# Kernel tuning notes

Hardware: AMD Instinct MI355X
Metric: run time of the kernel (lower is better)

Reference implementation:

```python
import jax, jax.numpy as jnp
import numpy as np

B, S, D, H, DK = 32, 1024, 256, 8, 32
MASK_VALUE = -1e-30  # note: NOT -inf; masked scores become ~0 pre-softmax, faithful to source


def setup_inputs() -> dict:
    key = jax.random.key(0)
    ks = jax.random.split(key, 7)
    query = jax.random.normal(ks[0], (B, S, D), dtype=jnp.float32)
    key_t = jax.random.normal(ks[1], (B, S, D), dtype=jnp.float32)
    value = jax.random.normal(ks[2], (B, S, D), dtype=jnp.float32)
    # binary observation mask over key positions
    mask = (jax.random.uniform(ks[3], (B, S)) > 0.5).astype(jnp.float32)
    glorot = jax.nn.initializers.glorot_uniform(in_axis=1, out_axis=2)
    Wq = glorot(ks[4], (H, D, DK), jnp.float32)
    Wk = glorot(ks[5], (H, D, DK), jnp.float32)
    Wv = glorot(ks[6], (H, D, DK), jnp.float32)
    return {"query": query, "key": key_t, "value": value, "mask": mask,
            "Wq": Wq, "Wk": Wk, "Wv": Wv}


def reference(query, key, value, mask, Wq, Wk, Wv):
    # per-head projections, vectorized over heads: [B,S,D] x [H,D,DK] -> [B,H,S,DK]
    q = jnp.einsum('bsd,hdk->bhsk', query, Wq)
    k = jnp.einsum('bsd,hdk->bhsk', key, Wk)
    v = jnp.einsum('bsd,hdk->bhsk', value, Wv)
    # raw scores (no 1/sqrt(dk) scaling in source): [B,H,Sq,Sk]
    A = jnp.einsum('bhqk,bhsk->bhqs', q, k)
    m = mask[:, None, None, :]  # [B,1,1,Sk]
    A = m * A + (1.0 - m) * MASK_VALUE  # multiplicative mask, NOT additive
    A = jax.nn.softmax(A, axis=-1)
    out = jnp.einsum('bhqs,bhsk->bhqk', A, v)  # [B,H,Sq,DK]
    # concat heads along last dim, matching torch.cat order
    return out.transpose(0, 2, 1, 3).reshape(B, S, H * DK)
```

## Files before the change

### kernel.cpp

```cpp
#include <hip/hip_runtime.h>
#include <math.h>

#define B_  32
#define S_  1024
#define D_  256
#define H_  8
#define DK_ 32
#define MASKV (-1e-30f)
#define LOG2E 1.44269504f

typedef __attribute__((ext_vector_type(4))) short bf4_t;
typedef __attribute__((ext_vector_type(8))) short bf8_t;
typedef __attribute__((ext_vector_type(4))) float f4_t;

__device__ __forceinline__ unsigned fbits(float x) {
    union { float f; unsigned u; } v; v.f = x; return v.u;
}
__device__ __forceinline__ float bitsf(unsigned u) {
    union { unsigned u; float f; } v; v.u = u; return v.f;
}

#if __has_builtin(__builtin_amdgcn_exp2f)
#define EXP2F(x) __builtin_amdgcn_exp2f(x)
#else
#define EXP2F(x) __expf((x) * 0.69314718f)
#endif

__device__ __forceinline__ void gld16(const void* g, void* l) {
    __builtin_amdgcn_global_load_lds(
        (const __attribute__((address_space(1))) void*)g,
        (__attribute__((address_space(3))) void*)l, 16, 0, 0);
}

#define PSEL 0x07060302u


__global__ __launch_bounds__(256) void prep_w(
    const float* __restrict__ Wq, const float* __restrict__ Wk,
    const float* __restrict__ Wv, short* __restrict__ WpH, short* __restrict__ WpL)
{
    const int a = blockIdx.x >> 3;
    const int h = blockIdx.x & 7;
    const float* W = (a == 0 ? Wq : (a == 1 ? Wk : Wv)) + (size_t)h * 256 * 32;
    const int t = threadIdx.x;
    const int k    = t & 31;
    const int dgrp = t >> 5;
    const int ng   = h * 2 + (k >> 4);
    const int l15  = k & 15;
#pragma unroll
    for (int jj = blockIdx.y * 2; jj < blockIdx.y * 2 + 2; ++jj) {
        const int d0 = jj * 32 + dgrp * 4;
        float x[4];
#pragma unroll
        for (int r = 0; r < 4; ++r) x[r] = W[(size_t)(d0 + r) * 32 + k];
        unsigned hu[4], lu[4];
#pragma unroll
        for (int r = 0; r < 4; ++r) {
            unsigned hb = (fbits(x[r]) + 0x8000u) & 0xFFFF0000u;
            hu[r] = hb;
            lu[r] = fbits(x[r] - bitsf(hb)) + 0x8000u;
        }
        uint2 hp = make_uint2(__builtin_amdgcn_perm(hu[1], hu[0], PSEL),
                              __builtin_amdgcn_perm(hu[3], hu[2], PSEL));
        uint2 lp = make_uint2(__builtin_amdgcn_perm(lu[1], lu[0], PSEL),
                              __builtin_amdgcn_perm(lu[3], lu[2], PSEL));
        const int quad = (d0 >> 3) & 3;
        const int jb   = d0 & 7;
        size_t off = (size_t)a * 65536
                   + ((size_t)(jj * 16 + ng) * 64 + quad * 16 + l15) * 8 + jb;
        *(uint2*)&WpH[off] = hp;
        *(uint2*)&WpL[off] = lp;
    }
}

__global__ __launch_bounds__(256) void proj_kernel(
    const float* __restrict__ Xq, const float* __restrict__ Xk,
    const float* __restrict__ Xv, const float* __restrict__ mask,
    const short* __restrict__ WpH, const short* __restrict__ WpL,
    short* __restrict__ qpH, short* __restrict__ qpL,
    short* __restrict__ kpH, short* __restrict__ kpL,
    short* __restrict__ vpT)
{
    __shared__ __align__(16) short XsH[8192];
    __shared__ __align__(16) short XsL[8192];

    const int a  = blockIdx.y;
    const float* X = (a == 0 ? Xq : (a == 1 ? Xk : Xv));
    const short* WH = WpH + (size_t)a * 65536;
    const short* WL = WpL + (size_t)a * 65536;
    const int m0 = blockIdx.x * 64;

    const int tid  = threadIdx.x;
    const int lane = tid & 63;
    const int wv   = tid >> 6;
    const int l15  = lane & 15;
    const int quad = lane >> 4;

    f4_t acc[4][4];
#pragma unroll
    for (int i = 0; i < 4; ++i)
#pragma unroll
        for (int j = 0; j < 4; ++j) acc[i][j] = (f4_t){0.f, 0.f, 0.f, 0.f};

    const int r    = tid >> 2;
    const int dseg = tid & 3;
    const int tix  = r >> 4;
    const int rl15 = r & 15;

    for (int h2 = 0; h2 < 2; ++h2) {
        __syncthreads();
        {
            const float* xp = X + (size_t)(m0 + r) * 256 + h2 * 128 + dseg * 32;
#pragma unroll
            for (int q = 0; q < 4; ++q) {
                float4 x0 = *(const float4*)(xp + q * 8);
                float4 x1 = *(const float4*)(xp + q * 8 + 4);
                float xv[8] = {x0.x, x0.y, x0.z, x0.w, x1.x, x1.y, x1.z, x1.w};
                bf8_t hi, lo;
#pragma unroll
                for (int j = 0; j < 8; ++j) {
                    unsigned hu = (fbits(xv[j]) + 0x8000u) & 0xFFFF0000u;
                    hi[j] = (short)(hu >> 16);
                    lo[j] = (short)((fbits(xv[j] - bitsf(hu)) + 0x8000u) >> 16);
                }
                const int off = ((dseg * 4 + tix) * 64 + q * 16 + rl15) * 8;
                *(bf8_t*)&XsH[off] = hi;
                *(bf8_t*)&XsL[off] = lo;
            }
        }
        __syncthreads();

#pragma unroll
        for (int kcl = 0; kcl < 4; ++kcl) {
            const int kc = h2 * 4 + kcl;
            bf8_t xH[4], xL[4];
#pragma unroll
            for (int t = 0; t < 4; ++t) {
                xH[t] = *(const bf8_t*)&XsH[((kcl * 4 + t) * 64 + lane) * 8];
                xL[t] = *(const bf8_t*)&XsL[((kcl * 4 + t) * 64 + lane) * 8];
            }
#pragma unroll
            for (int ns = 0; ns < 4; ++ns) {
                const size_t wo = ((size_t)(kc * 16 + wv * 4 + ns) * 64 + lane) * 8;
                bf8_t wh = *(const bf8_t*)&WH[wo];
                bf8_t wl = *(const bf8_t*)&WL[wo];
#pragma unroll
                for (int t = 0; t < 4; ++t) {
                    f4_t c = acc[t][ns];
                    if (a < 2) {
                        c = __builtin_amdgcn_mfma_f32_16x16x32_bf16(wh, xH[t], c, 0, 0, 0);
                        c = __builtin_amdgcn_mfma_f32_16x16x32_bf16(wl, xH[t], c, 0, 0, 0);
                        c = __builtin_amdgcn_mfma_f32_16x16x32_bf16(wh, xL[t], c, 0, 0, 0);
                    } else {
                        c = __builtin_amdgcn_mfma_f32_16x16x32_bf16(xH[t], wh, c, 0, 0, 0);
                        c = __builtin_amdgcn_mfma_f32_16x16x32_bf16(xH[t], wl, c, 0, 0, 0);
                        c = __builtin_amdgcn_mfma_f32_16x16x32_bf16(xL[t], wh, c, 0, 0, 0);
                    }
                    acc[t][ns] = c;
                }
            }
        }
    }

    const int b  = m0 >> 10;
    const int sB = m0 & 1023;
    if (a < 2) {
        short* dH = (a == 0) ? qpH : kpH;
        short* dL = (a == 0) ? qpL : kpL;
        const float* mbp = mask + (size_t)b * 1024;
#pragma unroll
        for (int t = 0; t < 4; ++t) {
            const int s = sB + t * 16 + l15;
            const float scale = (a == 0) ? LOG2E : mbp[s];
            const int grp = (sB >> 4) + t;
#pragma unroll
            for (int ns = 0; ns < 4; ++ns) {
                const int h_    = wv * 2 + (ns >> 1);
                const int quadA = (ns & 1) * 2 + (quad >> 1);
                const int jb    = (quad & 1) * 4;
                unsigned hu[4], lu[4];
#pragma unroll
                for (int rr = 0; rr < 4; ++rr) {
                    float x = acc[t][ns][rr] * scale;
                    unsigned h32 = fbits(x) + 0x8000u;
                    hu[rr] = h32;
                    float hf = bitsf(h32 & 0xFFFF0000u);
                    lu[rr] = fbits(x - hf) + 0x8000u;
                }
                uint2 hp = make_uint2(__builtin_amdgcn_perm(hu[1], hu[0], PSEL),
                                      __builtin_amdgcn_perm(hu[3], hu[2], PSEL));
                uint2 lp = make_uint2(__builtin_amdgcn_perm(lu[1], lu[0], PSEL),
                                      __builtin_amdgcn_perm(lu[3], lu[2], PSEL));
                size_t off = (((size_t)(b * 8 + h_) * 64 + grp) * 64
                              + quadA * 16 + l15) * 8 + jb;
                *(uint2*)&dH[off] = hp;
                *(uint2*)&dL[off] = lp;
            }
        }
    } else {
#pragma unroll
        for (int t = 0; t < 4; ++t) {
            int sr = sB + t * 16 + quad * 4;
#pragma unroll
            for (int ns = 0; ns < 4; ++ns) {
                int n = wv * 64 + ns * 16 + l15;
                int h = n >> 5, k = n & 31;
                unsigned eu[4];
#pragma unroll
                for (int rr = 0; rr < 4; ++rr) eu[rr] = fbits(acc[t][ns][rr]) + 0x8000u;
                uint2 pk = make_uint2(__builtin_amdgcn_perm(eu[1], eu[0], PSEL),
                                      __builtin_amdgcn_perm(eu[3], eu[2], PSEL));
                *(uint2*)&vpT[((size_t)(b * 8 + h) * 32 + k) * 1024 + sr] = pk;
            }
        }
    }
}

__global__ __launch_bounds__(256) void attn_kernel(
    const short* __restrict__ qpH, const short* __restrict__ qpL,
    const short* __restrict__ kpH, const short* __restrict__ kpL,
    const short* __restrict__ vpT, float* __restrict__ out)
{
    __shared__ __align__(16) short KsH[2][2048];
    __shared__ __align__(16) short KsL[2][2048];
    __shared__ __align__(16) short VsT[2][32 * 72];

    const int tid  = threadIdx.x;
    const int lane = tid & 63;
    const int wv   = tid >> 6;
    const int l15  = lane & 15;
    const int quad = lane >> 4;

    const int L  = (blockIdx.z * gridDim.y + blockIdx.y) * gridDim.x + blockIdx.x;
    const int li = L >> 3;
    const int bh = (L & 7) * 32 + (li >> 3);
    const int qt = li & 7;
    const int b  = bh >> 3;
    const int h  = bh & 7;
    const int woff = qt * 128 + wv * 32;

    bf8_t qh[2], ql[2];
#pragma unroll
    for (int qs = 0; qs < 2; ++qs) {
        const int grp = qt * 8 + wv * 2 + qs;
        size_t off = (((size_t)bh * 64 + grp) * 64 + lane) * 8;
        qh[qs] = *(const bf8_t*)&qpH[off];
        ql[qs] = *(const bf8_t*)&qpL[off];
    }

    f4_t accO[2][2];
    f4_t accS[2];
#pragma unroll
    for (int i = 0; i < 2; ++i) {
        accS[i] = (f4_t){0.f, 0.f, 0.f, 0.f};
#pragma unroll
        for (int j = 0; j < 2; ++j) accO[i][j] = (f4_t){0.f, 0.f, 0.f, 0.f};
    }
    const bf4_t ones4 = {(short)0x3F80, (short)0x3F80, (short)0x3F80, (short)0x3F80};

    const int dv = tid >> 3, seg = tid & 7;

    {
        size_t toff = ((size_t)bh * 64) * 512;
        gld16(kpH + toff + wv * 512 + lane * 8, (char*)KsH[0] + wv * 1024);
        gld16(kpL + toff + wv * 512 + lane * 8, (char*)KsL[0] + wv * 1024);
        uint4 v0 = *(const uint4*)&vpT[((size_t)bh * 32 + dv) * 1024 + seg * 8];
        *(uint4*)&VsT[0][dv * 72 + seg * 8] = v0;
    }
    __syncthreads();

    int cur = 0;
    for (int kt = 0; kt < 16; ++kt) {
        const int nxt = cur ^ 1;

        uint4 vreg;
        if (kt < 15) {
            size_t toff = ((size_t)bh * 64 + (kt + 1) * 4) * 512;
            gld16(kpH + toff + wv * 512 + lane * 8, (char*)KsH[nxt] + wv * 1024);
            gld16(kpL + toff + wv * 512 + lane * 8, (char*)KsL[nxt] + wv * 1024);
            vreg = *(const uint4*)&vpT[((size_t)bh * 32 + dv) * 1024 + (kt + 1) * 64 + seg * 8];
        }

        __builtin_amdgcn_s_setprio(1);
        f4_t sc[2][4];
#pragma unroll
        for (int ks = 0; ks < 4; ++ks) {
            bf8_t kh = *(const bf8_t*)&KsH[cur][ks * 512 + lane * 8];
            bf8_t kl = *(const bf8_t*)&KsL[cur][ks * 512 + lane * 8];
#pragma unroll
            for (int qs = 0; qs < 2; ++qs) {
                f4_t c = __builtin_amdgcn_mfma_f32_16x16x32_bf16(kh, qh[qs],
                             (f4_t){0.f, 0.f, 0.f, 0.f}, 0, 0, 0);
                c = __builtin_amdgcn_mfma_f32_16x16x32_bf16(kl, qh[qs], c, 0, 0, 0);
                c = __builtin_amdgcn_mfma_f32_16x16x32_bf16(kh, ql[qs], c, 0, 0, 0);
                sc[qs][ks] = c;
            }
        }

        bf4_t pf[2][4];
#pragma unroll
        for (int ks = 0; ks < 4; ++ks) {
#pragma unroll
            for (int qs = 0; qs < 2; ++qs) {
                unsigned eu[4];
#pragma unroll
                for (int r = 0; r < 4; ++r)
                    eu[r] = fbits(EXP2F(sc[qs][ks][r])) + 0x8000u;
                union { uint2 u; bf4_t v; } cv;
                cv.u = make_uint2(__builtin_amdgcn_perm(eu[1], eu[0], PSEL),
                                  __builtin_amdgcn_perm(eu[3], eu[2], PSEL));
                pf[qs][ks] = cv.v;
            }
        }

#pragma unroll
        for (int ks = 0; ks < 4; ++ks) {
            bf4_t vf0 = *(const bf4_t*)&VsT[cur][l15 * 72 + ks * 16 + quad * 4];
            bf4_t vf1 = *(const bf4_t*)&VsT[cur][(16 + l15) * 72 + ks * 16 + quad * 4];
#pragma unroll
            for (int qs = 0; qs < 2; ++qs) {
                accO[qs][0] = __builtin_amdgcn_mfma_f32_16x16x16bf16_1k(vf0, pf[qs][ks], accO[qs][0], 0, 0, 0);
                accO[qs][1] = __builtin_amdgcn_mfma_f32_16x16x16bf16_1k(vf1, pf[qs][ks], accO[qs][1], 0, 0, 0);
                accS[qs]    = __builtin_amdgcn_mfma_f32_16x16x16bf16_1k(ones4, pf[qs][ks], accS[qs], 0, 0, 0);
            }
        }
        __builtin_amdgcn_s_setprio(0);

        if (kt < 15) *(uint4*)&VsT[nxt][dv * 72 + seg * 8] = vreg;
        __syncthreads();
        cur = nxt;
    }

#pragma unroll
    for (int qs = 0; qs < 2; ++qs) {
        float inv = 1.0f / accS[qs][0];
        int s = woff + qs * 16 + l15;
        float* op = out + ((size_t)b * 1024 + s) * 256 + h * 32;
#pragma unroll
        for (int dvs = 0; dvs < 2; ++dvs) {
            float4 o4 = make_float4(accO[qs][dvs][0] * inv, accO[qs][dvs][1] * inv,
                                    accO[qs][dvs][2] * inv, accO[qs][dvs][3] * inv);
            *(float4*)&op[dvs * 16 + quad * 4] = o4;
        }
    }
}

extern "C" void kernel_launch(void* const* d_in, const int* in_sizes, int n_in,
                              void* d_out, int out_size, void* d_ws, size_t ws_size,
                              hipStream_t stream)
{
    const float* query = (const float*)d_in[0];
    const float* key   = (const float*)d_in[1];
    const float* value = (const float*)d_in[2];
    const float* mask  = (const float*)d_in[3];
    const float* Wq    = (const float*)d_in[4];
    const float* Wk    = (const float*)d_in[5];
    const float* Wv    = (const float*)d_in[6];
    float* out = (float*)d_out;

    const size_t per = (size_t)B_ * H_ * S_ * DK_;
    short* qpH = (short*)d_ws;
    short* qpL = qpH + per;
    short* kpH = qpL + per;
    short* kpL = kpH + per;
    short* vpT = kpL + per;
    short* WpH = vpT + per;
    short* WpL = WpH + 3 * 256 * 256;

    prep_w<<<dim3(24, 4), 256, 0, stream>>>(Wq, Wk, Wv, WpH, WpL);
    proj_kernel<<<dim3(512, 3), 256, 0, stream>>>(query, key, value, mask, WpH, WpL,
                                                  qpH, qpL, kpH, kpL, vpT);
    attn_kernel<<<dim3(8, H_, B_), 256, 0, stream>>>(qpH, qpL, kpH, kpL, vpT, out);
}
```

Measured before the change: 277.0 us.

## Software-pipeline attention loop so PV MFMAs of previous tile overlap QK and exp

Restructures the key-tile loop as a macro-unrolled, two-stage software pipeline. While the QK^T MFMAs for tile kt run, the P·V and row-sum MFMAs for tile kt-1 are issued, with that tile's V fragments and bf16 probabilities kept in ping-pong registers. A final drain step handles the last tile. The aim is to hide the exp and bf16-pack VALU work and the MFMA dependency latency behind independent matrix work, at the cost of more live registers and a fully unrolled, larger code body.

After: 271.9 us. Within noise of the previous version (-1.8%).

```diff
diff --git a/kernel.cpp b/kernel.cpp
--- a/kernel.cpp
+++ b/kernel.cpp
@@ -260,6 +260,70 @@
 
     const int dv = tid >> 3, seg = tid & 7;
 
+    bf4_t vA[8], vB[8];
+    bf4_t pfA[2][4], pfB[2][4];
+
+#define TILE(KT, CUR, DO_STAGE, DO_PV, VIN, VOUT, PIN, POUT)                    \
+    {                                                                           \
+                      \
+        _Pragma("unroll")                                                       \
+        for (int ks = 0; ks < 4; ++ks) {                                        \
+            VOUT[ks * 2]     = *(const bf4_t*)&VsT[CUR][l15 * 72 + ks * 16 + quad * 4];       \
+            VOUT[ks * 2 + 1] = *(const bf4_t*)&VsT[CUR][(16 + l15) * 72 + ks * 16 + quad * 4];\
+        }                                                                       \
+                    \
+        uint4 vreg;                                                             \
+        if (DO_STAGE) {                                                         \
+            size_t toff = ((size_t)bh * 64 + (size_t)((KT) + 1) * 4) * 512;     \
+            gld16(kpH + toff + wv * 512 + lane * 8, (char*)KsH[(CUR) ^ 1] + wv * 1024); \
+            gld16(kpL + toff + wv * 512 + lane * 8, (char*)KsL[(CUR) ^ 1] + wv * 1024); \
+            vreg = *(const uint4*)&vpT[((size_t)bh * 32 + dv) * 1024            \
+                                       + (size_t)((KT) + 1) * 64 + seg * 8];    \
+        }                                                                       \
+        __builtin_amdgcn_s_setprio(1);                                          \
+                       \
+        _Pragma("unroll")                                                       \
+        for (int ks = 0; ks < 4; ++ks) {                                        \
+            bf8_t kh = *(const bf8_t*)&KsH[CUR][ks * 512 + lane * 8];           \
+            bf8_t kl = *(const bf8_t*)&KsL[CUR][ks * 512 + lane * 8];           \
+            f4_t sc[2];                                                         \
+            _Pragma("unroll")                                                   \
+            for (int qs = 0; qs < 2; ++qs) {                                    \
+                f4_t c = __builtin_amdgcn_mfma_f32_16x16x32_bf16(kh, qh[qs],    \
+                             (f4_t){0.f, 0.f, 0.f, 0.f}, 0, 0, 0);              \
+                c = __builtin_amdgcn_mfma_f32_16x16x32_bf16(kl, qh[qs], c, 0, 0, 0); \
+                c = __builtin_amdgcn_mfma_f32_16x16x32_bf16(kh, ql[qs], c, 0, 0, 0); \
+                sc[qs] = c;                                                     \
+            }                                                                   \
+            if (DO_PV) {                                                        \
+                _Pragma("unroll")                                               \
+                for (int qs = 0; qs < 2; ++qs) {                                \
+                    accO[qs][0] = __builtin_amdgcn_mfma_f32_16x16x16bf16_1k(    \
+                                      VIN[ks * 2], PIN[qs][ks], accO[qs][0], 0, 0, 0);     \
+                    accO[qs][1] = __builtin_amdgcn_mfma_f32_16x16x16bf16_1k(    \
+                                      VIN[ks * 2 + 1], PIN[qs][ks], accO[qs][1], 0, 0, 0); \
+                    accS[qs]    = __builtin_amdgcn_mfma_f32_16x16x16bf16_1k(    \
+                                      ones4, PIN[qs][ks], accS[qs], 0, 0, 0);   \
+                }                                                               \
+            }                                                                   \
+            _Pragma("unroll")                                                   \
+            for (int qs = 0; qs < 2; ++qs) {                                    \
+                unsigned eu[4];                                                 \
+                _Pragma("unroll")                                               \
+                for (int r = 0; r < 4; ++r)                                     \
+                    eu[r] = fbits(EXP2F(sc[qs][r])) + 0x8000u;                  \
+                union { uint2 u; bf4_t v; } cv;                                 \
+                cv.u = make_uint2(__builtin_amdgcn_perm(eu[1], eu[0], PSEL),    \
+                                  __builtin_amdgcn_perm(eu[3], eu[2], PSEL));   \
+                POUT[qs][ks] = cv.v;                                            \
+            }                                                                   \
+        }                                                                       \
+        __builtin_amdgcn_s_setprio(0);                                          \
+                 \
+        if (DO_STAGE) *(uint4*)&VsT[(CUR) ^ 1][dv * 72 + seg * 8] = vreg;       \
+        __syncthreads();                                                        \
+    }
+
     {
         size_t toff = ((size_t)bh * 64) * 512;
         gld16(kpH + toff + wv * 512 + lane * 8, (char*)KsH[0] + wv * 1024);
@@ -269,67 +333,26 @@
     }
     __syncthreads();
 
-    int cur = 0;
-    for (int kt = 0; kt < 16; ++kt) {
-        const int nxt = cur ^ 1;
-
-        uint4 vreg;
-        if (kt < 15) {
-            size_t toff = ((size_t)bh * 64 + (kt + 1) * 4) * 512;
-            gld16(kpH + toff + wv * 512 + lane * 8, (char*)KsH[nxt] + wv * 1024);
-            gld16(kpL + toff + wv * 512 + lane * 8, (char*)KsL[nxt] + wv * 1024);
-            vreg = *(const uint4*)&vpT[((size_t)bh * 32 + dv) * 1024 + (kt + 1) * 64 + seg * 8];
-        }
-
-        __builtin_amdgcn_s_setprio(1);
-        f4_t sc[2][4];
-#pragma unroll
-        for (int ks = 0; ks < 4; ++ks) {
-            bf8_t kh = *(const bf8_t*)&KsH[cur][ks * 512 + lane * 8];
-            bf8_t kl = *(const bf8_t*)&KsL[cur][ks * 512 + lane * 8];
-#pragma unroll
-            for (int qs = 0; qs < 2; ++qs) {
-                f4_t c = __builtin_amdgcn_mfma_f32_16x16x32_bf16(kh, qh[qs],
-                             (f4_t){0.f, 0.f, 0.f, 0.f}, 0, 0, 0);
-                c = __builtin_amdgcn_mfma_f32_16x16x32_bf16(kl, qh[qs], c, 0, 0, 0);
-                c = __builtin_amdgcn_mfma_f32_16x16x32_bf16(kh, ql[qs], c, 0, 0, 0);
-                sc[qs][ks] = c;
-            }
-        }
-
-        bf4_t pf[2][4];
-#pragma unroll
-        for (int ks = 0; ks < 4; ++ks) {
-#pragma unroll
-            for (int qs = 0; qs < 2; ++qs) {
-                unsigned eu[4];
-#pragma unroll
-                for (int r = 0; r < 4; ++r)
-                    eu[r] = fbits(EXP2F(sc[qs][ks][r])) + 0x8000u;
-                union { uint2 u; bf4_t v; } cv;
-                cv.u = make_uint2(__builtin_amdgcn_perm(eu[1], eu[0], PSEL),
-                                  __builtin_amdgcn_perm(eu[3], eu[2], PSEL));
-                pf[qs][ks] = cv.v;
-            }
-        }
-
-#pragma unroll
-        for (int ks = 0; ks < 4; ++ks) {
-            bf4_t vf0 = *(const bf4_t*)&VsT[cur][l15 * 72 + ks * 16 + quad * 4];
-            bf4_t vf1 = *(const bf4_t*)&VsT[cur][(16 + l15) * 72 + ks * 16 + quad * 4];
-#pragma unroll
-            for (int qs = 0; qs < 2; ++qs) {
-                accO[qs][0] = __builtin_amdgcn_mfma_f32_16x16x16bf16_1k(vf0, pf[qs][ks], accO[qs][0], 0, 0, 0);
-                accO[qs][1] = __builtin_amdgcn_mfma_f32_16x16x16bf16_1k(vf1, pf[qs][ks], accO[qs][1], 0, 0, 0);
-                accS[qs]    = __builtin_amdgcn_mfma_f32_16x16x16bf16_1k(ones4, pf[qs][ks], accS[qs], 0, 0, 0);
-            }
-        }
-        __builtin_amdgcn_s_setprio(0);
-
-        if (kt < 15) *(uint4*)&VsT[nxt][dv * 72 + seg * 8] = vreg;
-        __syncthreads();
-        cur = nxt;
-    }
+    TILE(0, 0, 1, 0, vA, vA, pfA, pfA)
+    for (int i = 0; i < 7; ++i) {
+        TILE(2 * i + 1, 1, 1, 1, vA, vB, pfA, pfB)
+        TILE(2 * i + 2, 0, 1, 1, vB, vA, pfB, pfA)
+    }
+    TILE(15, 1, 0, 1, vA, vB, pfA, pfB)
+
+#pragma unroll
+    for (int ks = 0; ks < 4; ++ks) {
+#pragma unroll
+        for (int qs = 0; qs < 2; ++qs) {
+            accO[qs][0] = __builtin_amdgcn_mfma_f32_16x16x16bf16_1k(
+                              vB[ks * 2], pfB[qs][ks], accO[qs][0], 0, 0, 0);
+            accO[qs][1] = __builtin_amdgcn_mfma_f32_16x16x16bf16_1k(
+                              vB[ks * 2 + 1], pfB[qs][ks], accO[qs][1], 0, 0, 0);
+            accS[qs]    = __builtin_amdgcn_mfma_f32_16x16x16bf16_1k(
+                              ones4, pfB[qs][ks], accS[qs], 0, 0, 0);
+        }
+    }
+#undef TILE
 
 #pragma unroll
     for (int qs = 0; qs < 2; ++qs) {
```
